# Kernel tuning notes

Hardware: AMD Instinct MI355X
Metric: run time of the kernel (lower is better)

Reference implementation:

```python
import jax, jax.numpy as jnp
import numpy as np

B, L, D = 8, 2048, 64

def setup_inputs() -> dict:
    key = jax.random.key(0)
    kq, kk, kv, kqm, kkm = jax.random.split(key, 5)
    return {
        "query": jax.random.normal(kq, (B, L, D), dtype=jnp.float32),
        "key": jax.random.normal(kk, (B, L, D), dtype=jnp.float32),
        "value": jax.random.normal(kv, (B, L, D), dtype=jnp.float32),
        "q_mask": jax.random.randint(kqm, (B, L), 0, 2, dtype=jnp.int32),
        "k_mask": jax.random.randint(kkm, (B, L), 0, 2, dtype=jnp.int32),
    }

def reference(query, key, value, q_mask, k_mask):
    # scale defaults to D_q; divide scores by sqrt(D_q)
    D_q = query.shape[-1]
    qm = q_mask.astype(jnp.float32)  # [B, L_q]
    km = k_mask.astype(jnp.float32)  # [B, L_k]
    # outer-product mask: [B, L_q, L_k]
    mask = qm[:, :, None] * km[:, None, :]
    scores = jnp.einsum("bqd,bkd->bqk", query, key) / jnp.sqrt(jnp.float32(D_q))
    # masked_fill(-inf).exp(): masked positions become exactly 0
    A = jnp.where(mask == 0, 0.0, jnp.exp(scores))  # [B, L_q, L_k]
    # sum clamped to min 1.0 (NOT a standard softmax normalization)
    A_sum = jnp.maximum(A.sum(axis=-1, keepdims=True), 1.0)
    attn = A / A_sum
    return jnp.einsum("bqk,bkd->bqd", attn, value)
```

## Files before the change

kernel.cpp:

```cpp
#include <hip/hip_runtime.h>
#include <hip/hip_bf16.h>
#include <stdint.h>

#define BB 8
#define LL 2048
#define DD 64

typedef short bf16x8 __attribute__((ext_vector_type(8)));
typedef float f32x4 __attribute__((ext_vector_type(4)));
typedef unsigned short ushort_t;
typedef __attribute__((address_space(1))) const unsigned int gas_u32;
typedef __attribute__((address_space(3))) unsigned int las_u32;

__device__ __forceinline__ unsigned pk2(float lo, float hi) {
    union { __hip_bfloat162 h; unsigned u; } c;
    c.h = __float22bfloat162_rn(make_float2(lo, hi));
    return c.u;
}
__device__ __forceinline__ float4 ld4(const float* __restrict__ p) {
    return *reinterpret_cast<const float4*>(p);
}
__device__ __forceinline__ bf16x8 cvt8f(float4 a, float4 b) {
    union { bf16x8 v; unsigned u[4]; } r;
    r.u[0] = pk2(a.x, a.y); r.u[1] = pk2(a.z, a.w);
    r.u[2] = pk2(b.x, b.y); r.u[3] = pk2(b.z, b.w);
    return r.v;
}
__device__ __forceinline__ void glds16(const void* g, void* lds_base_uniform) {
    __builtin_amdgcn_global_load_lds((gas_u32*)g, (las_u32*)lds_base_uniform, 16, 0, 0);
}
__device__ __forceinline__ unsigned f2bf_u(float f) {
    union { float f; unsigned u; } v; v.f = f;
    return (v.u + 0x8000u) >> 16;
}
__device__ __forceinline__ bf16x8 cvt8(const float* __restrict__ p) {
    float4 a = ld4(p), b = ld4(p + 4);
    union { bf16x8 v; unsigned u[4]; } r;
    r.u[0] = f2bf_u(a.x) | (f2bf_u(a.y) << 16);
    r.u[1] = f2bf_u(a.z) | (f2bf_u(a.w) << 16);
    r.u[2] = f2bf_u(b.x) | (f2bf_u(b.y) << 16);
    r.u[3] = f2bf_u(b.z) | (f2bf_u(b.w) << 16);
    return r.v;
}

__global__ __launch_bounds__(256) void pack_k_bf16(const float* __restrict__ K,
                                                   ushort_t* __restrict__ Kb) {
    size_t i = ((size_t)blockIdx.x * 256 + threadIdx.x) * 8;
    float4 a = ld4(K + i), b = ld4(K + i + 4);
    uint4 o = { pk2(a.x, a.y), pk2(a.z, a.w), pk2(b.x, b.y), pk2(b.z, b.w) };
    *reinterpret_cast<uint4*>(Kb + i) = o;
}

__global__ __launch_bounds__(256) void transpose_v_bf(const float* __restrict__ V,
                                                      ushort_t* __restrict__ VT) {
    __shared__ float t[64][65];
    const int b  = blockIdx.x >> 5;
    const int kt = (blockIdx.x & 31) << 6;
    {
        const int r  = threadIdx.x >> 2;
        const int cq = (threadIdx.x & 3) << 4;
        const float* src = V + ((size_t)(b * LL + kt + r)) * DD + cq;
        #pragma unroll
        for (int i = 0; i < 4; ++i) {
            float4 v = ld4(src + 4 * i);
            t[r][cq + 4 * i + 0] = v.x; t[r][cq + 4 * i + 1] = v.y;
            t[r][cq + 4 * i + 2] = v.z; t[r][cq + 4 * i + 3] = v.w;
        }
    }
    __syncthreads();
    {
        const int d  = threadIdx.x >> 2;
        const int kq = (threadIdx.x & 3) << 4;
        ushort_t* dst = VT + ((size_t)(b * DD + d)) * LL + kt + kq;
        #pragma unroll
        for (int u = 0; u < 2; ++u) {
            uint4 o;
            o.x = pk2(t[kq + 8 * u + 0][d], t[kq + 8 * u + 1][d]);
            o.y = pk2(t[kq + 8 * u + 2][d], t[kq + 8 * u + 3][d]);
            o.z = pk2(t[kq + 8 * u + 4][d], t[kq + 8 * u + 5][d]);
            o.w = pk2(t[kq + 8 * u + 6][d], t[kq + 8 * u + 7][d]);
            *reinterpret_cast<uint4*>(dst + 8 * u) = o;
        }
    }
}

__global__ __launch_bounds__(512, 1) void attn5(
    const float* __restrict__ Q,
    const ushort_t* __restrict__ Kbf,
    const ushort_t* __restrict__ VTb,
    const int* __restrict__ qmask,
    const int* __restrict__ kmask,
    float* __restrict__ Out)
{
    const int tid  = threadIdx.x;
    const int wave = tid >> 6;
    const int lane = tid & 63;
    const int ln   = lane & 15;
    const int quad = lane >> 4;
    const int s    = wave >> 1;
    const int h    = wave & 1;

    const int b  = blockIdx.x >> 5;
    const int q0 = (blockIdx.x & 31) << 6;

    __shared__ char  ldsbuf[2][16384];
    __shared__ float kmf[LL];
    __shared__ float Osum[64][68];
    __shared__ float Dsum[64];

    for (int i = tid; i < 64 * 68; i += 512) (&Osum[0][0])[i] = 0.f;
    if (tid < 64) Dsum[tid] = 0.f;
    {
        int4 m = *reinterpret_cast<const int4*>(kmask + b * LL + tid * 4);
        float4 f = { (float)m.x, (float)m.y, (float)m.z, (float)m.w };
        *reinterpret_cast<float4*>(&kmf[tid * 4]) = f;
    }

    bf16x8 qf[2];
    {
        const float* qp = Q + ((size_t)(b * LL + q0 + 16 * s + ln)) * DD + quad * 8;
        qf[0] = cvt8f(ld4(qp),      ld4(qp + 4));
        qf[1] = cvt8f(ld4(qp + 32), ld4(qp + 36));
    }

    const char* Kg = (const char*)Kbf + (size_t)b * LL * DD * 2;
    const char* Vg = (const char*)VTb + (size_t)b * DD * LL * 2;
    const int g  = wave * 64 + lane;
    const int rS = g >> 3;
    const int cS = (g & 7) ^ (rS & 7);

    f32x4 Oacc[4] = {{0,0,0,0},{0,0,0,0},{0,0,0,0},{0,0,0,0}};
    float dsum = 0.f;

    const int src0 = ln + ((quad & 1) << 5);
    const int src1 = src0 + 16;
    const bool hi  = quad >= 2;

    #define STAGE(buf, k0)                                                        \
        do {                                                                      \
            glds16(Kg + (size_t)((k0) + rS) * 128 + cS * 16,                      \
                   &ldsbuf[buf][wave * 1024]);                                    \
            glds16(Vg + (size_t)rS * (LL * 2) + (k0) * 2 + cS * 16,               \
                   &ldsbuf[buf][8192 + wave * 1024]);                             \
        } while (0)

    STAGE(0, 0);

    for (int i = 0; i < 32; ++i) {
        __syncthreads();
        const int knext = ((i + 1) & 31) * 64;
        STAGE((i + 1) & 1, knext);

        const int   k0 = i * 64;
        const char* LK = ldsbuf[i & 1];
        const char* LV = ldsbuf[i & 1] + 8192;

        bf16x8 kf[2][2];
        #pragma unroll
        for (int tt = 0; tt < 2; ++tt) {
            const int r = 16 * (2 * h + tt) + ln;
            #pragma unroll
            for (int dh = 0; dh < 2; ++dh) {
                const int c = (dh * 4 + quad) ^ (ln & 7);
                kf[tt][dh] = *reinterpret_cast<const bf16x8*>(LK + r * 128 + c * 16);
            }
        }
        bf16x8 vf[4];
        const int cv = (4 * h + quad) ^ (ln & 7);
        #pragma unroll
        for (int db = 0; db < 4; ++db) {
            const int d = db * 16 + ln;
            vf[db] = *reinterpret_cast<const bf16x8*>(LV + d * 128 + cv * 16);
        }

        unsigned w[2][2];
        #pragma unroll
        for (int tt = 0; tt < 2; ++tt) {
            f32x4 acc = (f32x4){0.f, 0.f, 0.f, 0.f};
            acc = __builtin_amdgcn_mfma_f32_16x16x32_bf16(kf[tt][0], qf[0], acc, 0, 0, 0);
            acc = __builtin_amdgcn_mfma_f32_16x16x32_bf16(kf[tt][1], qf[1], acc, 0, 0, 0);
            const float4 km = *reinterpret_cast<const float4*>(
                &kmf[k0 + 16 * (2 * h + tt) + 4 * quad]);
            float e0 = __expf(acc[0] * 0.125f) * km.x;
            float e1 = __expf(acc[1] * 0.125f) * km.y;
            float e2 = __expf(acc[2] * 0.125f) * km.z;
            float e3 = __expf(acc[3] * 0.125f) * km.w;
            dsum += (e0 + e1) + (e2 + e3);
            w[tt][0] = pk2(e0, e1);
            w[tt][1] = pk2(e2, e3);
        }
        union { bf16x8 v; unsigned u[4]; } pf;
        {
            unsigned a0 = __shfl(w[0][0], src0), b0 = __shfl(w[1][0], src0);
            unsigned a1 = __shfl(w[0][1], src0), b1 = __shfl(w[1][1], src0);
            unsigned a2 = __shfl(w[0][0], src1), b2 = __shfl(w[1][0], src1);
            unsigned a3 = __shfl(w[0][1], src1), b3 = __shfl(w[1][1], src1);
            pf.u[0] = hi ? b0 : a0;
            pf.u[1] = hi ? b1 : a1;
            pf.u[2] = hi ? b2 : a2;
            pf.u[3] = hi ? b3 : a3;
        }
        #pragma unroll
        for (int db = 0; db < 4; ++db)
            Oacc[db] = __builtin_amdgcn_mfma_f32_16x16x32_bf16(pf.v, vf[db], Oacc[db], 0, 0, 0);
    }
    #undef STAGE

    {
        float v = dsum;
        v += __shfl_xor(v, 16);
        v += __shfl_xor(v, 32);
        dsum = v;
    }

    #pragma unroll
    for (int db = 0; db < 4; ++db)
        #pragma unroll
        for (int r = 0; r < 4; ++r)
            atomicAdd(&Osum[16 * s + quad * 4 + r][db * 16 + ln], Oacc[db][r]);
    if (quad == 0) atomicAdd(&Dsum[16 * s + ln], dsum);
    __syncthreads();

    const int q  = tid >> 3;
    const int d0 = (tid & 7) << 3;
    float dn  = Dsum[q];
    float inv = 1.0f / fmaxf(dn, 1.0f);
    float sc  = qmask[b * LL + q0 + q] ? inv : 0.0f;
    f32x4 o0 = *reinterpret_cast<const f32x4*>(&Osum[q][d0])     * sc;
    f32x4 o1 = *reinterpret_cast<const f32x4*>(&Osum[q][d0 + 4]) * sc;
    float* op = Out + ((size_t)(b * LL + q0 + q)) * DD + d0;
    *reinterpret_cast<f32x4*>(op)     = o0;
    *reinterpret_cast<f32x4*>(op + 4) = o1;
}

__global__ __launch_bounds__(256, 4) void attn_mfma(
    const float* __restrict__ Q, const float* __restrict__ K,
    const float* __restrict__ V, const int* __restrict__ qmask,
    const int* __restrict__ kmask, float* __restrict__ Out)
{
    const int tid  = threadIdx.x;
    const int wave = tid >> 6;
    const int lane = tid & 63;
    const int n    = lane & 15;
    const int quad = lane >> 4;
    const int bx = blockIdx.x;
    const int b  = bx >> 7;
    const int q0 = (bx & 127) << 4;
    __shared__ float Pl[4][576];
    __shared__ float Opart[4][16][68];
    __shared__ float Denp[4][16];
    const float* Qp = Q + ((size_t)(b * LL + q0 + n)) * DD + quad * 8;
    bf16x8 qf0 = cvt8(Qp);
    bf16x8 qf1 = cvt8(Qp + 32);
    const float* Kb = K + ((size_t)(b * LL) + n) * DD + quad * 8;
    const float* Vb = V + ((size_t)(b * LL) + quad * 8) * DD + n;
    const int* kmb = kmask + b * LL;
    f32x4 Oacc[4] = {{0,0,0,0},{0,0,0,0},{0,0,0,0},{0,0,0,0}};
    float den[4]  = {0.f, 0.f, 0.f, 0.f};
    float*       pw = &Pl[wave][144 * (n >> 3) + 36 * quad + (n & 7)];
    const float* pr = &Pl[wave][9 * lane];
    const int kbeg = wave * (LL / 4);
    const int kend = kbeg + (LL / 4);
    for (int k0 = kbeg; k0 < kend; k0 += 32) {
        const float* krow = Kb + (size_t)k0 * DD;
        bf16x8 kA0 = cvt8(krow);
        bf16x8 kA1 = cvt8(krow + 32);
        bf16x8 kB0 = cvt8(krow + 16 * DD);
        bf16x8 kB1 = cvt8(krow + 16 * DD + 32);
        f32x4 z = {0.f, 0.f, 0.f, 0.f};
        f32x4 S0 = __builtin_amdgcn_mfma_f32_16x16x32_bf16(qf0, kA0, z, 0, 0, 0);
        S0 = __builtin_amdgcn_mfma_f32_16x16x32_bf16(qf1, kA1, S0, 0, 0, 0);
        f32x4 S1 = __builtin_amdgcn_mfma_f32_16x16x32_bf16(qf0, kB0, z, 0, 0, 0);
        S1 = __builtin_amdgcn_mfma_f32_16x16x32_bf16(qf1, kB1, S1, 0, 0, 0);
        float km0 = (float)kmb[k0 + n];
        float km1 = (float)kmb[k0 + 16 + n];
        #pragma unroll
        for (int r = 0; r < 4; ++r) {
            float e0 = __expf(S0[r] * 0.125f) * km0;
            float e1 = __expf(S1[r] * 0.125f) * km1;
            den[r] += e0 + e1;
            pw[9 * r]       = e0;
            pw[288 + 9 * r] = e1;
        }
        __builtin_amdgcn_wave_barrier();
        float pv[8];
        #pragma unroll
        for (int j = 0; j < 8; ++j) pv[j] = pr[j];
        __builtin_amdgcn_wave_barrier();
        union { bf16x8 v; unsigned u[4]; } pf;
        #pragma unroll
        for (int j = 0; j < 4; ++j)
            pf.u[j] = f2bf_u(pv[2 * j]) | (f2bf_u(pv[2 * j + 1]) << 16);
        const float* vrow = Vb + (size_t)k0 * DD;
        #pragma unroll
        for (int db = 0; db < 4; ++db) {
            union { bf16x8 v; unsigned u[4]; } vfr;
            #pragma unroll
            for (int jj = 0; jj < 4; ++jj) {
                unsigned lo  = f2bf_u(vrow[(2 * jj) * DD + db * 16]);
                unsigned hi2 = f2bf_u(vrow[(2 * jj + 1) * DD + db * 16]);
                vfr.u[jj] = lo | (hi2 << 16);
            }
            Oacc[db] = __builtin_amdgcn_mfma_f32_16x16x32_bf16(pf.v, vfr.v, Oacc[db], 0, 0, 0);
        }
    }
    #pragma unroll
    for (int r = 0; r < 4; ++r) {
        float v = den[r];
        v += __shfl_xor(v, 1); v += __shfl_xor(v, 2);
        v += __shfl_xor(v, 4); v += __shfl_xor(v, 8);
        den[r] = v;
    }
    #pragma unroll
    for (int db = 0; db < 4; ++db)
        #pragma unroll
        for (int r = 0; r < 4; ++r)
            Opart[wave][quad * 4 + r][db * 16 + n] = Oacc[db][r];
    if (n == 0) {
        #pragma unroll
        for (int r = 0; r < 4; ++r) Denp[wave][quad * 4 + r] = den[r];
    }
    __syncthreads();
    const int q  = tid >> 4;
    const int d0 = (tid & 15) * 4;
    f32x4 sum = *reinterpret_cast<const f32x4*>(&Opart[0][q][d0]);
    sum += *reinterpret_cast<const f32x4*>(&Opart[1][q][d0]);
    sum += *reinterpret_cast<const f32x4*>(&Opart[2][q][d0]);
    sum += *reinterpret_cast<const f32x4*>(&Opart[3][q][d0]);
    float dn  = Denp[0][q] + Denp[1][q] + Denp[2][q] + Denp[3][q];
    float inv = 1.0f / fmaxf(dn, 1.0f);
    float s   = qmask[b * LL + q0 + q] ? inv : 0.0f;
    f32x4 o   = sum * s;
    float* op = Out + ((size_t)(b * LL + q0 + q)) * DD + d0;
    *reinterpret_cast<f32x4*>(op) = o;
}

extern "C" void kernel_launch(void* const* d_in, const int* in_sizes, int n_in,
                              void* d_out, int out_size, void* d_ws, size_t ws_size,
                              hipStream_t stream) {
    (void)in_sizes; (void)n_in; (void)out_size;
    const float* Q  = (const float*)d_in[0];
    const float* K  = (const float*)d_in[1];
    const float* V  = (const float*)d_in[2];
    const int* qm   = (const int*)d_in[3];
    const int* km   = (const int*)d_in[4];
    float* Out      = (float*)d_out;

    const size_t elems    = (size_t)BB * LL * DD;
    const size_t ws_need  = elems * 2 * sizeof(ushort_t);
    if (ws_size >= ws_need && d_ws != nullptr) {
        ushort_t* Kbf = (ushort_t*)d_ws;
        ushort_t* VTb = Kbf + elems;
        pack_k_bf16   <<<dim3(elems / (256 * 8)), dim3(256), 0, stream>>>(K, Kbf);
        transpose_v_bf<<<dim3(BB * (LL / 64)),    dim3(256), 0, stream>>>(V, VTb);
        attn5<<<dim3(BB * (LL / 64)), dim3(512), 0, stream>>>(Q, Kbf, VTb, qm, km, Out);
    } else {
        attn_mfma<<<dim3(BB * (LL / 16)), dim3(256), 0, stream>>>(Q, K, V, qm, km, Out);
    }
}
```

Baseline: 112.8 us.

## Rebalance attention kernel to 32-query blocks with 128-key tiles and bf16 mask

The attention kernel now gives each block 32 queries instead of 64, doubling the grid to 512 blocks. Each block splits keys across four wave groups per query slice and stages 128-key tiles, so the loop runs 16 times instead of 32 and the barrier count halves. The key mask is stored in LDS as bf16 to shrink shared memory, exp is computed as exp2 with a folded scale, and the launch bound is raised to allow several blocks per CU. In exchange, more blocks each re-load and re-convert the full K/V stream, which doubles K/V traffic per query, and per-tile LDS use grows.

After: 117.5 us. +4.2%, slower.

```diff
diff --git a/kernel.cpp b/kernel.cpp
--- a/kernel.cpp
+++ b/kernel.cpp
@@ -28,6 +28,9 @@
 }
 __device__ __forceinline__ void glds16(const void* g, void* lds_base_uniform) {
     __builtin_amdgcn_global_load_lds((gas_u32*)g, (las_u32*)lds_base_uniform, 16, 0, 0);
+}
+__device__ __forceinline__ float bfu2f(unsigned bits) {
+    union { unsigned u; float f; } c; c.u = bits << 16; return c.f;
 }
 __device__ __forceinline__ unsigned f2bf_u(float f) {
     union { float f; unsigned u; } v; v.f = f;
@@ -84,7 +87,7 @@
     }
 }
 
-__global__ __launch_bounds__(512, 1) void attn5(
+__global__ __launch_bounds__(512, 4) void attn7(
     const float* __restrict__ Q,
     const ushort_t* __restrict__ Kbf,
     const ushort_t* __restrict__ VTb,
@@ -97,25 +100,47 @@
     const int lane = tid & 63;
     const int ln   = lane & 15;
     const int quad = lane >> 4;
-    const int s    = wave >> 1;
-    const int h    = wave & 1;
-
-    const int b  = blockIdx.x >> 5;
-    const int q0 = (blockIdx.x & 31) << 6;
-
-    __shared__ char  ldsbuf[2][16384];
-    __shared__ float kmf[LL];
-    __shared__ float Osum[64][68];
-    __shared__ float Dsum[64];
-
-    for (int i = tid; i < 64 * 68; i += 512) (&Osum[0][0])[i] = 0.f;
-    if (tid < 64) Dsum[tid] = 0.f;
-    {
-        int4 m = *reinterpret_cast<const int4*>(kmask + b * LL + tid * 4);
-        float4 f = { (float)m.x, (float)m.y, (float)m.z, (float)m.w };
-        *reinterpret_cast<float4*>(&kmf[tid * 4]) = f;
-    }
-
+    const int s    = wave >> 2;
+    const int h    = wave & 3;
+
+    const int b  = blockIdx.x >> 6;
+    const int q0 = (blockIdx.x & 63) << 5;
+
+    __shared__ char     lds[2][32768];
+    __shared__ ushort_t kmbf[LL];
+    __shared__ float    Osum[32][68];
+    __shared__ float    Dsum[32];
+
+    const char* Kg = (const char*)Kbf + (size_t)b * LL * DD * 2;
+    const char* Vg = (const char*)VTb + (size_t)b * DD * LL * 2;
+    const int krow1 = wave * 8 + (lane >> 3);
+    const int kscol = (lane & 7) ^ (lane >> 3);
+    const int vd1   = wave * 4 + (lane >> 4);
+    const int vscol = (lane & 15) ^ (vd1 & 15);
+
+    #define STAGE(buf, k0)                                                      \
+        do {                                                                    \
+            glds16(Kg + (size_t)((k0) + krow1) * 128 + kscol * 16,              \
+                   &lds[buf][wave * 1024]);                                     \
+            glds16(Kg + (size_t)((k0) + krow1 + 64) * 128 + kscol * 16,         \
+                   &lds[buf][(wave + 8) * 1024]);                               \
+            glds16(Vg + (size_t)vd1 * (LL * 2) + (k0) * 2 + vscol * 16,         \
+                   &lds[buf][16384 + wave * 1024]);                             \
+            glds16(Vg + (size_t)(vd1 + 32) * (LL * 2) + (k0) * 2 + vscol * 16,  \
+                   &lds[buf][16384 + (wave + 8) * 1024]);                       \
+        } while (0)
+
+    STAGE(0, 0);
+
+    for (int i = tid; i < 32 * 68; i += 512) (&Osum[0][0])[i] = 0.f;
+    if (tid < 32) Dsum[tid] = 0.f;
+    {
+        int4 a = *reinterpret_cast<const int4*>(kmask + b * LL + tid * 4);
+        uint2 u;
+        u.x = (a.x ? 0x3F80u : 0u) | ((a.y ? 0x3F80u : 0u) << 16);
+        u.y = (a.z ? 0x3F80u : 0u) | ((a.w ? 0x3F80u : 0u) << 16);
+        *reinterpret_cast<uint2*>(kmbf + tid * 4) = u;
+    }
     bf16x8 qf[2];
     {
         const float* qp = Q + ((size_t)(b * LL + q0 + 16 * s + ln)) * DD + quad * 8;
@@ -123,42 +148,26 @@
         qf[1] = cvt8f(ld4(qp + 32), ld4(qp + 36));
     }
 
-    const char* Kg = (const char*)Kbf + (size_t)b * LL * DD * 2;
-    const char* Vg = (const char*)VTb + (size_t)b * DD * LL * 2;
-    const int g  = wave * 64 + lane;
-    const int rS = g >> 3;
-    const int cS = (g & 7) ^ (rS & 7);
-
     f32x4 Oacc[4] = {{0,0,0,0},{0,0,0,0},{0,0,0,0},{0,0,0,0}};
     float dsum = 0.f;
 
     const int src0 = ln + ((quad & 1) << 5);
     const int src1 = src0 + 16;
     const bool hi  = quad >= 2;
-
-    #define STAGE(buf, k0)                                                        \
-        do {                                                                      \
-            glds16(Kg + (size_t)((k0) + rS) * 128 + cS * 16,                      \
-                   &ldsbuf[buf][wave * 1024]);                                    \
-            glds16(Vg + (size_t)rS * (LL * 2) + (k0) * 2 + cS * 16,               \
-                   &ldsbuf[buf][8192 + wave * 1024]);                             \
-        } while (0)
-
-    STAGE(0, 0);
-
-    for (int i = 0; i < 32; ++i) {
+    const float EC = 0.125f * 1.44269504f;
+
+    for (int it = 0; it < 16; ++it) {
         __syncthreads();
-        const int knext = ((i + 1) & 31) * 64;
-        STAGE((i + 1) & 1, knext);
-
-        const int   k0 = i * 64;
-        const char* LK = ldsbuf[i & 1];
-        const char* LV = ldsbuf[i & 1] + 8192;
+        if (it != 15) STAGE((it + 1) & 1, (it + 1) * 128);
+
+        const int   k0 = it * 128;
+        const char* LK = lds[it & 1];
+        const char* LV = lds[it & 1] + 16384;
 
         bf16x8 kf[2][2];
         #pragma unroll
         for (int tt = 0; tt < 2; ++tt) {
-            const int r = 16 * (2 * h + tt) + ln;
+            const int r = 32 * h + 16 * tt + ln;
             #pragma unroll
             for (int dh = 0; dh < 2; ++dh) {
                 const int c = (dh * 4 + quad) ^ (ln & 7);
@@ -166,11 +175,18 @@
             }
         }
         bf16x8 vf[4];
-        const int cv = (4 * h + quad) ^ (ln & 7);
         #pragma unroll
         for (int db = 0; db < 4; ++db) {
             const int d = db * 16 + ln;
-            vf[db] = *reinterpret_cast<const bf16x8*>(LV + d * 128 + cv * 16);
+            const int c = (4 * h + quad) ^ ln;
+            vf[db] = *reinterpret_cast<const bf16x8*>(LV + d * 256 + c * 16);
+        }
+        float4 fm[2];
+        #pragma unroll
+        for (int tt = 0; tt < 2; ++tt) {
+            ushort4 mu = *reinterpret_cast<const ushort4*>(
+                kmbf + k0 + 32 * h + 16 * tt + 4 * quad);
+            fm[tt] = make_float4(bfu2f(mu.x), bfu2f(mu.y), bfu2f(mu.z), bfu2f(mu.w));
         }
 
         unsigned w[2][2];
@@ -179,12 +195,10 @@
             f32x4 acc = (f32x4){0.f, 0.f, 0.f, 0.f};
             acc = __builtin_amdgcn_mfma_f32_16x16x32_bf16(kf[tt][0], qf[0], acc, 0, 0, 0);
             acc = __builtin_amdgcn_mfma_f32_16x16x32_bf16(kf[tt][1], qf[1], acc, 0, 0, 0);
-            const float4 km = *reinterpret_cast<const float4*>(
-                &kmf[k0 + 16 * (2 * h + tt) + 4 * quad]);
-            float e0 = __expf(acc[0] * 0.125f) * km.x;
-            float e1 = __expf(acc[1] * 0.125f) * km.y;
-            float e2 = __expf(acc[2] * 0.125f) * km.z;
-            float e3 = __expf(acc[3] * 0.125f) * km.w;
+            float e0 = exp2f(acc[0] * EC) * fm[tt].x;
+            float e1 = exp2f(acc[1] * EC) * fm[tt].y;
+            float e2 = exp2f(acc[2] * EC) * fm[tt].z;
+            float e3 = exp2f(acc[3] * EC) * fm[tt].w;
             dsum += (e0 + e1) + (e2 + e3);
             w[tt][0] = pk2(e0, e1);
             w[tt][1] = pk2(e2, e3);
@@ -221,16 +235,14 @@
     if (quad == 0) atomicAdd(&Dsum[16 * s + ln], dsum);
     __syncthreads();
 
-    const int q  = tid >> 3;
-    const int d0 = (tid & 7) << 3;
+    const int q  = tid >> 4;
+    const int d0 = (tid & 15) << 2;
     float dn  = Dsum[q];
     float inv = 1.0f / fmaxf(dn, 1.0f);
     float sc  = qmask[b * LL + q0 + q] ? inv : 0.0f;
-    f32x4 o0 = *reinterpret_cast<const f32x4*>(&Osum[q][d0])     * sc;
-    f32x4 o1 = *reinterpret_cast<const f32x4*>(&Osum[q][d0 + 4]) * sc;
+    f32x4 o = *reinterpret_cast<const f32x4*>(&Osum[q][d0]) * sc;
     float* op = Out + ((size_t)(b * LL + q0 + q)) * DD + d0;
-    *reinterpret_cast<f32x4*>(op)     = o0;
-    *reinterpret_cast<f32x4*>(op + 4) = o1;
+    *reinterpret_cast<f32x4*>(op) = o;
 }
 
 __global__ __launch_bounds__(256, 4) void attn_mfma(
@@ -353,7 +365,7 @@
         ushort_t* VTb = Kbf + elems;
         pack_k_bf16   <<<dim3(elems / (256 * 8)), dim3(256), 0, stream>>>(K, Kbf);
         transpose_v_bf<<<dim3(BB * (LL / 64)),    dim3(256), 0, stream>>>(V, VTb);
-        attn5<<<dim3(BB * (LL / 64)), dim3(512), 0, stream>>>(Q, Kbf, VTb, qm, km, Out);
+        attn7<<<dim3(BB * (LL / 32)), dim3(512), 0, stream>>>(Q, Kbf, VTb, qm, km, Out);
     } else {
         attn_mfma<<<dim3(BB * (LL / 16)), dim3(256), 0, stream>>>(Q, K, V, qm, km, Out);
     }
```
